# Optimization experiments

Measured on AMD Instinct MI355X. Metric: run time of the kernel, lower is better.

## Reference

```python
import jax, jax.numpy as jnp
import numpy as np

N_NODES = 50000
N_EDGES = 600000
D_FT = 128   # prompt_dim == node feature dim
D_E = 32     # edge feature dim


def setup_inputs() -> dict:
    key = jax.random.key(0)
    k1, k2, k3, k4, k5 = jax.random.split(key, 5)
    graph_embedding = jax.random.normal(k1, (N_NODES, D_FT), dtype=jnp.float32)
    e_feat = jax.random.normal(k2, (N_EDGES, D_E), dtype=jnp.float32)
    weight = jax.random.normal(k3, (1, D_FT), dtype=jnp.float32)  # learned prompt
    src_idx = jax.random.randint(k4, (N_EDGES,), 0, N_NODES)
    dst_idx = jax.random.randint(k5, (N_EDGES,), 0, N_NODES)
    return {"graph_embedding": graph_embedding, "e_feat": e_feat,
            "weight": weight, "src_idx": src_idx, "dst_idx": dst_idx}


def reference(graph_embedding, e_feat, weight, src_idx, dst_idx):
    # message m = concat(src_ft * p, e); dst_ft = segment_sum(m over dst).
    # concat commutes with segment-sum, so reduce the two halves separately
    # and concatenate at node level (avoids materializing [E, D_FT+D_E]).
    src_ft = graph_embedding[src_idx] * weight            # [E, D_FT]
    agg_ft = jax.ops.segment_sum(src_ft, dst_idx, num_segments=N_NODES)
    agg_e = jax.ops.segment_sum(e_feat, dst_idx, num_segments=N_NODES)
    return jnp.concatenate([agg_ft, agg_e], axis=1)      # [N, D_FT+D_E]
```

## Files before the change

### kernel.cpp

```cpp
#include <hip/hip_runtime.h>


#define D_FT 128
#define D_E 32
#define D_OUT (D_FT + D_E)
#define CAP 32

typedef float f32x4 __attribute__((ext_vector_type(4)));
typedef int   i32x2 __attribute__((ext_vector_type(2)));

__global__ void place_bucket_kernel(const int* __restrict__ src_idx,
                                    const int* __restrict__ dst_idx,
                                    int* __restrict__ cursor,
                                    i32x2* __restrict__ bucket,
                                    int* __restrict__ ovf,
                                    int* __restrict__ ovf_cnt, int E) {
    int i = blockIdx.x * blockDim.x + threadIdx.x;
    if (i >= E) return;
    int d = dst_idx[i];
    int slot = atomicAdd(&cursor[d], 1);
    if (slot < CAP) {
        i32x2 pr; pr.x = src_idx[i]; pr.y = i;
        bucket[(size_t)d * CAP + slot] = pr;
    } else {
        int p = atomicAdd(ovf_cnt, 1);
        ovf[p] = i;
    }
}

__global__ void gather_bucket_kernel(const float* __restrict__ emb,
                                     const float* __restrict__ e_feat,
                                     const float* __restrict__ w,
                                     const int* __restrict__ cursor,
                                     const i32x2* __restrict__ bucket,
                                     float* __restrict__ out, int N) {
    int g = (blockIdx.x * blockDim.x + threadIdx.x) >> 6;
    if (g >= N) return;
    const int lane = threadIdx.x & 63;
    const int half = lane >> 5;
    const int q    = lane & 31;
    const int qg   = q >> 3;
    const int ql   = q & 7;

    i32x2 pr = __builtin_nontemporal_load(&bucket[(size_t)g * CAP + (lane & 31)]);
    int cnt = cursor[g];
    cnt = cnt > CAP ? CAP : cnt;

    float4 accft = make_float4(0.f, 0.f, 0.f, 0.f);
    float4 acce  = make_float4(0.f, 0.f, 0.f, 0.f);

    int i = 0;
    for (; i + 8 <= cnt; i += 8) {
        int b  = i + (half << 2);
        int s0 = __shfl(pr.x, b + 0, 64);
        int s1 = __shfl(pr.x, b + 1, 64);
        int s2 = __shfl(pr.x, b + 2, 64);
        int s3 = __shfl(pr.x, b + 3, 64);
        int ee = __shfl(pr.y, b + qg, 64);
        float4 v0 = *reinterpret_cast<const float4*>(emb + (size_t)s0 * D_FT + q * 4);
        float4 v1 = *reinterpret_cast<const float4*>(emb + (size_t)s1 * D_FT + q * 4);
        float4 v2 = *reinterpret_cast<const float4*>(emb + (size_t)s2 * D_FT + q * 4);
        float4 v3 = *reinterpret_cast<const float4*>(emb + (size_t)s3 * D_FT + q * 4);
        f32x4 a = __builtin_nontemporal_load(
            reinterpret_cast<const f32x4*>(e_feat + (size_t)ee * D_E + ql * 4));
        accft.x += (v0.x + v1.x) + (v2.x + v3.x);
        accft.y += (v0.y + v1.y) + (v2.y + v3.y);
        accft.z += (v0.z + v1.z) + (v2.z + v3.z);
        accft.w += (v0.w + v1.w) + (v2.w + v3.w);
        acce.x += a.x; acce.y += a.y; acce.z += a.z; acce.w += a.w;
    }
    if (i < cnt) {
        const int c1 = cnt - 1;
        int b  = i + (half << 2);
        int t0 = b + 0, t1 = b + 1, t2 = b + 2, t3 = b + 3, te = b + qg;
        int s0 = __shfl(pr.x, t0 < c1 ? t0 : c1, 64);
        int s1 = __shfl(pr.x, t1 < c1 ? t1 : c1, 64);
        int s2 = __shfl(pr.x, t2 < c1 ? t2 : c1, 64);
        int s3 = __shfl(pr.x, t3 < c1 ? t3 : c1, 64);
        int ee = __shfl(pr.y, te < c1 ? te : c1, 64);
        float4 v0 = *reinterpret_cast<const float4*>(emb + (size_t)s0 * D_FT + q * 4);
        float4 v1 = *reinterpret_cast<const float4*>(emb + (size_t)s1 * D_FT + q * 4);
        float4 v2 = *reinterpret_cast<const float4*>(emb + (size_t)s2 * D_FT + q * 4);
        float4 v3 = *reinterpret_cast<const float4*>(emb + (size_t)s3 * D_FT + q * 4);
        f32x4 a = __builtin_nontemporal_load(
            reinterpret_cast<const f32x4*>(e_feat + (size_t)ee * D_E + ql * 4));
        float m0 = (t0 < cnt) ? 1.f : 0.f;
        float m1 = (t1 < cnt) ? 1.f : 0.f;
        float m2 = (t2 < cnt) ? 1.f : 0.f;
        float m3 = (t3 < cnt) ? 1.f : 0.f;
        float me = (te < cnt) ? 1.f : 0.f;
        accft.x = fmaf(v0.x, m0, accft.x); accft.y = fmaf(v0.y, m0, accft.y);
        accft.z = fmaf(v0.z, m0, accft.z); accft.w = fmaf(v0.w, m0, accft.w);
        accft.x = fmaf(v1.x, m1, accft.x); accft.y = fmaf(v1.y, m1, accft.y);
        accft.z = fmaf(v1.z, m1, accft.z); accft.w = fmaf(v1.w, m1, accft.w);
        accft.x = fmaf(v2.x, m2, accft.x); accft.y = fmaf(v2.y, m2, accft.y);
        accft.z = fmaf(v2.z, m2, accft.z); accft.w = fmaf(v2.w, m2, accft.w);
        accft.x = fmaf(v3.x, m3, accft.x); accft.y = fmaf(v3.y, m3, accft.y);
        accft.z = fmaf(v3.z, m3, accft.z); accft.w = fmaf(v3.w, m3, accft.w);
        acce.x = fmaf(a.x, me, acce.x); acce.y = fmaf(a.y, me, acce.y);
        acce.z = fmaf(a.z, me, acce.z); acce.w = fmaf(a.w, me, acce.w);
    }

    accft.x += __shfl_xor(accft.x, 32, 64);
    accft.y += __shfl_xor(accft.y, 32, 64);
    accft.z += __shfl_xor(accft.z, 32, 64);
    accft.w += __shfl_xor(accft.w, 32, 64);
    acce.x += __shfl_xor(acce.x, 8, 64);
    acce.y += __shfl_xor(acce.y, 8, 64);
    acce.z += __shfl_xor(acce.z, 8, 64);
    acce.w += __shfl_xor(acce.w, 8, 64);
    acce.x += __shfl_xor(acce.x, 16, 64);
    acce.y += __shfl_xor(acce.y, 16, 64);
    acce.z += __shfl_xor(acce.z, 16, 64);
    acce.w += __shfl_xor(acce.w, 16, 64);
    acce.x += __shfl_xor(acce.x, 32, 64);
    acce.y += __shfl_xor(acce.y, 32, 64);
    acce.z += __shfl_xor(acce.z, 32, 64);
    acce.w += __shfl_xor(acce.w, 32, 64);

    if (half == 0) {
        float4 wv = *reinterpret_cast<const float4*>(w + q * 4);
        float* o = out + (size_t)g * D_OUT;
        f32x4 r; r.x = accft.x * wv.x; r.y = accft.y * wv.y;
                 r.z = accft.z * wv.z; r.w = accft.w * wv.w;
        __builtin_nontemporal_store(r, reinterpret_cast<f32x4*>(o + q * 4));
        if (q < 8) {
            f32x4 re; re.x = acce.x; re.y = acce.y; re.z = acce.z; re.w = acce.w;
            __builtin_nontemporal_store(re, reinterpret_cast<f32x4*>(o + D_FT + q * 4));
        }
    }
}

__global__ void ovf_scatter_kernel(const float* __restrict__ emb,
                                   const float* __restrict__ e_feat,
                                   const float* __restrict__ w,
                                   const int* __restrict__ src_idx,
                                   const int* __restrict__ dst_idx,
                                   const int* __restrict__ ovf,
                                   const int* __restrict__ ovf_cnt,
                                   float* __restrict__ out) {
    int n = *ovf_cnt;
    int total = n * 40;
    for (int t = blockIdx.x * blockDim.x + threadIdx.x; t < total;
         t += gridDim.x * blockDim.x) {
        int e = t / 40, slot = t % 40;
        int eid = ovf[e];
        int d = dst_idx[eid];
        float* o = out + (size_t)d * D_OUT;
        if (slot < 32) {
            int s = src_idx[eid];
            float4 v  = *reinterpret_cast<const float4*>(emb + (size_t)s * D_FT + slot * 4);
            float4 wv = *reinterpret_cast<const float4*>(w + slot * 4);
            atomicAdd(o + slot * 4 + 0, v.x * wv.x);
            atomicAdd(o + slot * 4 + 1, v.y * wv.y);
            atomicAdd(o + slot * 4 + 2, v.z * wv.z);
            atomicAdd(o + slot * 4 + 3, v.w * wv.w);
        } else {
            int qq = slot - 32;
            float4 ve = *reinterpret_cast<const float4*>(e_feat + (size_t)eid * D_E + qq * 4);
            atomicAdd(o + D_FT + qq * 4 + 0, ve.x);
            atomicAdd(o + D_FT + qq * 4 + 1, ve.y);
            atomicAdd(o + D_FT + qq * 4 + 2, ve.z);
            atomicAdd(o + D_FT + qq * 4 + 3, ve.w);
        }
    }
}

__global__ void scatter_ft_kernel(const float* __restrict__ emb, const float* __restrict__ w,
                                  const int* __restrict__ src_idx, const int* __restrict__ dst_idx,
                                  float* __restrict__ out, int n_items) {
    int idx = blockIdx.x * blockDim.x + threadIdx.x;
    if (idx >= n_items) return;
    int e = idx >> 5, q = idx & 31;
    int s = src_idx[e], d = dst_idx[e];
    const float4 v  = *reinterpret_cast<const float4*>(emb + (size_t)s * D_FT + q * 4);
    const float4 wv = *reinterpret_cast<const float4*>(w + q * 4);
    float* o = out + (size_t)d * D_OUT + q * 4;
    atomicAdd(o + 0, v.x * wv.x); atomicAdd(o + 1, v.y * wv.y);
    atomicAdd(o + 2, v.z * wv.z); atomicAdd(o + 3, v.w * wv.w);
}
__global__ void scatter_e_kernel(const float* __restrict__ e_feat, const int* __restrict__ dst_idx,
                                 float* __restrict__ out, int n_items) {
    int idx = blockIdx.x * blockDim.x + threadIdx.x;
    if (idx >= n_items) return;
    int e = idx >> 3, q = idx & 7;
    int d = dst_idx[e];
    const float4 v = *reinterpret_cast<const float4*>(e_feat + (size_t)e * D_E + q * 4);
    float* o = out + (size_t)d * D_OUT + D_FT + q * 4;
    atomicAdd(o + 0, v.x); atomicAdd(o + 1, v.y);
    atomicAdd(o + 2, v.z); atomicAdd(o + 3, v.w);
}

extern "C" void kernel_launch(void* const* d_in, const int* in_sizes, int n_in,
                              void* d_out, int out_size, void* d_ws, size_t ws_size,
                              hipStream_t stream) {
    const float* emb    = (const float*)d_in[0];
    const float* e_feat = (const float*)d_in[1];
    const float* w      = (const float*)d_in[2];
    const int*   src    = (const int*)d_in[3];
    const int*   dst    = (const int*)d_in[4];
    float* out = (float*)d_out;

    const int E = in_sizes[3];
    const int N = out_size / D_OUT;

    size_t ints_head = (size_t)N + 2;
    size_t need = ints_head * 4 + (size_t)N * CAP * 8 + (size_t)E * 4;

    if (ws_size >= need) {
        int*   cursor  = (int*)d_ws;
        int*   ovf_cnt = cursor + N;
        i32x2* bucket  = (i32x2*)(cursor + ints_head);
        int*   ovf     = (int*)(bucket + (size_t)N * CAP);

        hipMemsetAsync(cursor, 0, ints_head * sizeof(int), stream);
        place_bucket_kernel<<<(E + 255) / 256, 256, 0, stream>>>(
            src, dst, cursor, bucket, ovf, ovf_cnt, E);
        gather_bucket_kernel<<<((size_t)N * 64 + 255) / 256, 256, 0, stream>>>(
            emb, e_feat, w, cursor, bucket, out, N);
        ovf_scatter_kernel<<<128, 256, 0, stream>>>(
            emb, e_feat, w, src, dst, ovf, ovf_cnt, out);
    } else {
        hipMemsetAsync(d_out, 0, (size_t)out_size * sizeof(float), stream);
        int items_ft = E * 32, items_e = E * 8;
        scatter_ft_kernel<<<(items_ft + 255) / 256, 256, 0, stream>>>(emb, w, src, dst, out, items_ft);
        scatter_e_kernel<<<(items_e + 255) / 256, 256, 0, stream>>>(e_feat, dst, out, items_e);
    }
}
```

Baseline: 101.0 us.

## Restructure gather loop: 8 rows per half-wave, separate edge-feature loop, launch bounds

Each half-wave now gathers 8 source rows per iteration instead of 4, with a single masked loop body replacing the full-loop-plus-tail structure. The edge-feature accumulation moves into its own loop in which all 64 lanes, in 8 groups of 8, each fetch one edge row. The kernel also gets __launch_bounds__(256, 8). The goal is more memory-level parallelism per iteration and fewer iterations for the typical degree of about 12. The cost is more registers and masked wasted loads on partial iterations.

```diff
diff --git a/kernel.cpp b/kernel.cpp
--- a/kernel.cpp
+++ b/kernel.cpp
@@ -28,67 +28,56 @@
     }
 }
 
-__global__ void gather_bucket_kernel(const float* __restrict__ emb,
-                                     const float* __restrict__ e_feat,
-                                     const float* __restrict__ w,
-                                     const int* __restrict__ cursor,
-                                     const i32x2* __restrict__ bucket,
-                                     float* __restrict__ out, int N) {
+__global__ __launch_bounds__(256, 8)
+void gather_bucket_kernel(const float* __restrict__ emb,
+                          const float* __restrict__ e_feat,
+                          const float* __restrict__ w,
+                          const int* __restrict__ cursor,
+                          const i32x2* __restrict__ bucket,
+                          float* __restrict__ out, int N) {
     int g = (blockIdx.x * blockDim.x + threadIdx.x) >> 6;
     if (g >= N) return;
     const int lane = threadIdx.x & 63;
     const int half = lane >> 5;
     const int q    = lane & 31;
-    const int qg   = q >> 3;
-    const int ql   = q & 7;
+    const int sub  = lane >> 3;
+    const int ql8  = lane & 7;
 
     i32x2 pr = __builtin_nontemporal_load(&bucket[(size_t)g * CAP + (lane & 31)]);
     int cnt = cursor[g];
     cnt = cnt > CAP ? CAP : cnt;
+    const int c1 = cnt - 1;
 
     float4 accft = make_float4(0.f, 0.f, 0.f, 0.f);
-    float4 acce  = make_float4(0.f, 0.f, 0.f, 0.f);
-
-    int i = 0;
-    for (; i + 8 <= cnt; i += 8) {
-        int b  = i + (half << 2);
-        int s0 = __shfl(pr.x, b + 0, 64);
-        int s1 = __shfl(pr.x, b + 1, 64);
-        int s2 = __shfl(pr.x, b + 2, 64);
-        int s3 = __shfl(pr.x, b + 3, 64);
-        int ee = __shfl(pr.y, b + qg, 64);
+
+    for (int i = 0; i < cnt; i += 16) {
+        int b  = i + (half << 3);
+        int t0 = b + 0, t1 = b + 1, t2 = b + 2, t3 = b + 3;
+        int t4 = b + 4, t5 = b + 5, t6 = b + 6, t7 = b + 7;
+        int s0 = __shfl(pr.x, t0 < c1 ? t0 : c1, 64);
+        int s1 = __shfl(pr.x, t1 < c1 ? t1 : c1, 64);
+        int s2 = __shfl(pr.x, t2 < c1 ? t2 : c1, 64);
+        int s3 = __shfl(pr.x, t3 < c1 ? t3 : c1, 64);
+        int s4 = __shfl(pr.x, t4 < c1 ? t4 : c1, 64);
+        int s5 = __shfl(pr.x, t5 < c1 ? t5 : c1, 64);
+        int s6 = __shfl(pr.x, t6 < c1 ? t6 : c1, 64);
+        int s7 = __shfl(pr.x, t7 < c1 ? t7 : c1, 64);
         float4 v0 = *reinterpret_cast<const float4*>(emb + (size_t)s0 * D_FT + q * 4);
         float4 v1 = *reinterpret_cast<const float4*>(emb + (size_t)s1 * D_FT + q * 4);
         float4 v2 = *reinterpret_cast<const float4*>(emb + (size_t)s2 * D_FT + q * 4);
         float4 v3 = *reinterpret_cast<const float4*>(emb + (size_t)s3 * D_FT + q * 4);
-        f32x4 a = __builtin_nontemporal_load(
-            reinterpret_cast<const f32x4*>(e_feat + (size_t)ee * D_E + ql * 4));
-        accft.x += (v0.x + v1.x) + (v2.x + v3.x);
-        accft.y += (v0.y + v1.y) + (v2.y + v3.y);
-        accft.z += (v0.z + v1.z) + (v2.z + v3.z);
-        accft.w += (v0.w + v1.w) + (v2.w + v3.w);
-        acce.x += a.x; acce.y += a.y; acce.z += a.z; acce.w += a.w;
-    }
-    if (i < cnt) {
-        const int c1 = cnt - 1;
-        int b  = i + (half << 2);
-        int t0 = b + 0, t1 = b + 1, t2 = b + 2, t3 = b + 3, te = b + qg;
-        int s0 = __shfl(pr.x, t0 < c1 ? t0 : c1, 64);
-        int s1 = __shfl(pr.x, t1 < c1 ? t1 : c1, 64);
-        int s2 = __shfl(pr.x, t2 < c1 ? t2 : c1, 64);
-        int s3 = __shfl(pr.x, t3 < c1 ? t3 : c1, 64);
-        int ee = __shfl(pr.y, te < c1 ? te : c1, 64);
-        float4 v0 = *reinterpret_cast<const float4*>(emb + (size_t)s0 * D_FT + q * 4);
-        float4 v1 = *reinterpret_cast<const float4*>(emb + (size_t)s1 * D_FT + q * 4);
-        float4 v2 = *reinterpret_cast<const float4*>(emb + (size_t)s2 * D_FT + q * 4);
-        float4 v3 = *reinterpret_cast<const float4*>(emb + (size_t)s3 * D_FT + q * 4);
-        f32x4 a = __builtin_nontemporal_load(
-            reinterpret_cast<const f32x4*>(e_feat + (size_t)ee * D_E + ql * 4));
+        float4 v4 = *reinterpret_cast<const float4*>(emb + (size_t)s4 * D_FT + q * 4);
+        float4 v5 = *reinterpret_cast<const float4*>(emb + (size_t)s5 * D_FT + q * 4);
+        float4 v6 = *reinterpret_cast<const float4*>(emb + (size_t)s6 * D_FT + q * 4);
+        float4 v7 = *reinterpret_cast<const float4*>(emb + (size_t)s7 * D_FT + q * 4);
         float m0 = (t0 < cnt) ? 1.f : 0.f;
         float m1 = (t1 < cnt) ? 1.f : 0.f;
         float m2 = (t2 < cnt) ? 1.f : 0.f;
         float m3 = (t3 < cnt) ? 1.f : 0.f;
-        float me = (te < cnt) ? 1.f : 0.f;
+        float m4 = (t4 < cnt) ? 1.f : 0.f;
+        float m5 = (t5 < cnt) ? 1.f : 0.f;
+        float m6 = (t6 < cnt) ? 1.f : 0.f;
+        float m7 = (t7 < cnt) ? 1.f : 0.f;
         accft.x = fmaf(v0.x, m0, accft.x); accft.y = fmaf(v0.y, m0, accft.y);
         accft.z = fmaf(v0.z, m0, accft.z); accft.w = fmaf(v0.w, m0, accft.w);
         accft.x = fmaf(v1.x, m1, accft.x); accft.y = fmaf(v1.y, m1, accft.y);
@@ -97,6 +86,23 @@
         accft.z = fmaf(v2.z, m2, accft.z); accft.w = fmaf(v2.w, m2, accft.w);
         accft.x = fmaf(v3.x, m3, accft.x); accft.y = fmaf(v3.y, m3, accft.y);
         accft.z = fmaf(v3.z, m3, accft.z); accft.w = fmaf(v3.w, m3, accft.w);
+        accft.x = fmaf(v4.x, m4, accft.x); accft.y = fmaf(v4.y, m4, accft.y);
+        accft.z = fmaf(v4.z, m4, accft.z); accft.w = fmaf(v4.w, m4, accft.w);
+        accft.x = fmaf(v5.x, m5, accft.x); accft.y = fmaf(v5.y, m5, accft.y);
+        accft.z = fmaf(v5.z, m5, accft.z); accft.w = fmaf(v5.w, m5, accft.w);
+        accft.x = fmaf(v6.x, m6, accft.x); accft.y = fmaf(v6.y, m6, accft.y);
+        accft.z = fmaf(v6.z, m6, accft.z); accft.w = fmaf(v6.w, m6, accft.w);
+        accft.x = fmaf(v7.x, m7, accft.x); accft.y = fmaf(v7.y, m7, accft.y);
+        accft.z = fmaf(v7.z, m7, accft.z); accft.w = fmaf(v7.w, m7, accft.w);
+    }
+
+    float4 acce = make_float4(0.f, 0.f, 0.f, 0.f);
+    for (int i = 0; i < cnt; i += 8) {
+        int te = i + sub;
+        int ee = __shfl(pr.y, te < c1 ? te : c1, 64);
+        f32x4 a = __builtin_nontemporal_load(
+            reinterpret_cast<const f32x4*>(e_feat + (size_t)ee * D_E + ql8 * 4));
+        float me = (te < cnt) ? 1.f : 0.f;
         acce.x = fmaf(a.x, me, acce.x); acce.y = fmaf(a.y, me, acce.y);
         acce.z = fmaf(a.z, me, acce.z); acce.w = fmaf(a.w, me, acce.w);
     }
```

New measurement: 115.7 us. 14.5% more time.
